# Performance work log

Measured on AMD Instinct MI355X. Metric: run time of the kernel, lower is better.

## Reference

```python
import jax, jax.numpy as jnp
import numpy as np

EPS = 1e-12  # matches torch.nn.functional.normalize default eps

def _l2_normalize(x):
    # F.normalize: x / max(||x||_2, eps)
    n = jnp.sqrt(jnp.sum(x * x, axis=-1, keepdims=True))
    return x / jnp.maximum(n, EPS)

def setup_inputs() -> dict:
    key = jax.random.key(0)
    k1, k2, k3, k4, k5 = jax.random.split(key, 5)
    B, N, D, V = 2048, 50000, 256, 256
    return {
        "query": jax.random.normal(k1, (B, D), dtype=jnp.float32),
        "W": jax.random.normal(k2, (D, D), dtype=jnp.float32) * (1.0 / np.sqrt(D)),
        "b": jax.random.normal(k3, (D,), dtype=jnp.float32) * 0.01,
        "keys": jax.random.normal(k4, (N, D), dtype=jnp.float32),
        "values": jax.random.normal(k5, (N, V), dtype=jnp.float32),
        "usage": jnp.ones((N,), dtype=jnp.float32),
        "top_k": 8,
    }

def reference(query, W, b, keys, values, usage, top_k):
    # q = Linear(query)  (store is full: n_stored == capacity, so no padding branch)
    q = query @ W.T + b                      # (B, D)
    q_norm = _l2_normalize(q)                # (B, D)
    k_norm = _l2_normalize(keys)             # (N, D)
    sim = q_norm @ k_norm.T                  # (B, N) cosine similarity
    scores, indices = jax.lax.top_k(sim, top_k)   # (B, K), (B, K)
    retrieved_values = values[indices]       # (B, K, V) gather
    # usage counter update: +1 per retrieved index (duplicates accumulate)
    usage_new = usage.at[indices.reshape(-1)].add(1.0)
    return retrieved_values, scores, usage_new
```

## Files before the change

### kernel.cpp

```cpp
#include <hip/hip_runtime.h>

#define D 256
#define NKEYS 50000
#define KCHUNK 256
#define NCHUNK 196
#define NKPAD (KCHUNK * NCHUNK)
#define BQ 2048
#define NC (NCHUNK * 4)
#define NCAND 16
#define DNEG_INF (-1.0e300)

typedef __attribute__((ext_vector_type(8))) __bf16 bf16x8;
typedef __attribute__((ext_vector_type(16))) float f32x16;

__device__ __forceinline__ unsigned short f2bf(float x) {
  unsigned int u = __float_as_uint(x);
  unsigned int r = (u + 0x7fffu + ((u >> 16) & 1u)) >> 16;
  return (unsigned short)r;
}

__global__ __launch_bounds__(256) void prep_kernel(const float* __restrict__ query,
                                                   const float* __restrict__ W,
                                                   const float* __restrict__ b,
                                                   const float* __restrict__ keys,
                                                   const float* __restrict__ usage,
                                                   unsigned short* __restrict__ qbf,
                                                   double* __restrict__ q64n,
                                                   double* __restrict__ kinv64,
                                                   unsigned short* __restrict__ kbf,
                                                   float* __restrict__ out_u) {
  __shared__ __align__(16) float As[8][20];
  __shared__ __align__(16) float Bs[256][20];
  if (blockIdx.x < 256) {
    const int tid = threadIdx.x;
    const int qt = tid >> 5;
    const int nt = tid & 31;
    const int m0 = blockIdx.x * 8;

    double acc[8];
#pragma unroll
    for (int j = 0; j < 8; j++) acc[j] = 0.0;

    for (int k0 = 0; k0 < D; k0 += 16) {
      if (tid < 32) {
        int r = tid >> 2, f = tid & 3;
        *(float4*)(&As[r][f * 4]) = *(const float4*)(&query[(m0 + r) * D + k0 + f * 4]);
      }
#pragma unroll
      for (int i = 0; i < 4; i++) {
        int r = (tid >> 2) + 64 * i, f = tid & 3;
        *(float4*)(&Bs[r][f * 4]) = *(const float4*)(&W[r * D + k0 + f * 4]);
      }
      __syncthreads();
#pragma unroll
      for (int kk = 0; kk < 16; kk += 4) {
        float4 af = *(const float4*)(&As[qt][kk]);
#pragma unroll
        for (int j = 0; j < 8; j++) {
          float4 bf = *(const float4*)(&Bs[nt + 32 * j][kk]);
          acc[j] = fma((double)af.x, (double)bf.x, acc[j]);
          acc[j] = fma((double)af.y, (double)bf.y, acc[j]);
          acc[j] = fma((double)af.z, (double)bf.z, acc[j]);
          acc[j] = fma((double)af.w, (double)bf.w, acc[j]);
        }
      }
      __syncthreads();
    }
#pragma unroll
    for (int j = 0; j < 8; j++) acc[j] += (double)b[nt + 32 * j];

    double s = 0.0;
#pragma unroll
    for (int j = 0; j < 8; j++) s = fma(acc[j], acc[j], s);
#pragma unroll
    for (int m = 16; m; m >>= 1) s += __shfl_xor(s, m, 32);
    double den = fmax(sqrt(s), 1e-12);
    int row = m0 + qt;
#pragma unroll
    for (int j = 0; j < 8; j++) {
      double v = acc[j] / den;
      q64n[row * D + nt + 32 * j] = v;
      qbf[row * D + nt + 32 * j] = f2bf((float)v);
    }
  } else {
    int wave = threadIdx.x >> 6, lane = threadIdx.x & 63;
    int r = (blockIdx.x - 256) * 4 + wave;
    if (r >= NKPAD) return;
    if (lane == 0 && r < NKEYS) out_u[r] = usage[r];
    int e = lane * 4;
    int e2 = e ^ ((r & 31) << 3);
    unsigned short* dst = kbf + (long long)r * D + e2;
    if (r >= NKEYS) {
      ushort4 z = {0, 0, 0, 0};
      *(ushort4*)dst = z;
      return;
    }
    float4 v = *(const float4*)(&keys[(long long)r * D + e]);
    double s = (double)v.x * v.x + (double)v.y * v.y + (double)v.z * v.z + (double)v.w * v.w;
#pragma unroll
    for (int m = 32; m; m >>= 1) s += __shfl_xor(s, m, 64);
    double inv = 1.0 / fmax(sqrt(s), 1e-12);
    if (lane == 0) kinv64[r] = inv;
    float fi = (float)inv;
    ushort4 o;
    o.x = f2bf(v.x * fi); o.y = f2bf(v.y * fi); o.z = f2bf(v.z * fi); o.w = f2bf(v.w * fi);
    *(ushort4*)dst = o;
  }
}

__global__ __launch_bounds__(256, 4) void sim_mfma_kernel(const unsigned short* __restrict__ qbf,
                                                          const unsigned short* __restrict__ kbf,
                                                          unsigned int* __restrict__ cand_p) {
  __shared__ __align__(16) unsigned char klds[2][16384];
  const int bid = blockIdx.x;
  const int k8 = bid & 7;
  const int ii = bid >> 3;
  const int qt = ii & 15;
  const int chunk = (ii >> 4) * 8 + k8;
  if (chunk >= NCHUNK) return;
  const int n0 = chunk * KCHUNK;
  const int m0 = qt * 128;

  const int tid = threadIdx.x;
  const int w = tid >> 6;
  const int l = tid & 63;
  const int col = l & 31;
  const int hi = l >> 5;
  const int qrow = m0 + w * 32 + col;

  bf16x8 qf[16];
#pragma unroll
  for (int ks = 0; ks < 16; ks++)
    qf[ks] = *(const bf16x8*)(qbf + (long long)qrow * D + ks * 16 + hi * 8);

  unsigned int s0 = 0u, s1 = 0u, s2 = 0u, s3 = 0u;
  const bool edge = (n0 + KCHUNK > NKEYS);
  const int rbase = col * 512 + hi * 16;
  const int swz = col << 4;
  const char* kchunk = (const char*)kbf + (long long)n0 * 512;

  auto prefetch = [&](unsigned char* buf, int kst) {
#pragma unroll
    for (int i = 0; i < 4; i++) {
      int dstbase = i * 4096 + w * 1024;
      int off = dstbase + l * 16;
      const void* src = kchunk + (long long)(kst * 32 + (off >> 9)) * 512 + (off & 511);
      __builtin_amdgcn_global_load_lds(src, (void*)(buf + dstbase), 16, 0, 0);
    }
  };

  auto compute = [&](const unsigned char* buf, int st) {
    f32x16 acc;
#pragma unroll
    for (int r = 0; r < 16; r++) acc[r] = 0.f;
#pragma unroll
    for (int ks = 0; ks < 16; ks++) {
      bf16x8 a = *(const bf16x8*)(buf + ((rbase + ks * 32) ^ swz));
      acc = __builtin_amdgcn_mfma_f32_32x32x16_bf16(a, qf[ks], acc, 0, 0, 0);
    }
#pragma unroll
    for (int r = 0; r < 16; r++) {
      unsigned int u = __float_as_uint(acc[r] + 2.0f);
      int slot = st * 32 + (r & 3) + 8 * (r >> 2) + 4 * hi;
      unsigned int v = (u & 0xFFFFFF00u) | (unsigned)slot;
      if (edge && (n0 + slot >= NKEYS)) v = 0u;
      unsigned int a0 = min(s0, v); s0 = max(s0, v);
      unsigned int a1 = min(s1, a0); s1 = max(s1, a0);
      unsigned int a2 = min(s2, a1); s2 = max(s2, a1);
      s3 = max(s3, a2);
    }
  };

  prefetch(&klds[0][0], 0);
  __syncthreads();

#pragma unroll 1
  for (int st = 0; st < 8; st += 2) {
    prefetch(&klds[1][0], st + 1);
    compute(&klds[0][0], st);
    __syncthreads();
    if (st + 2 < 8) prefetch(&klds[0][0], st + 2);
    compute(&klds[1][0], st + 1);
    __syncthreads();
  }

  unsigned int b0 = (unsigned int)__shfl_xor((int)s0, 32, 64);
  unsigned int b1 = (unsigned int)__shfl_xor((int)s1, 32, 64);
  unsigned int b2 = (unsigned int)__shfl_xor((int)s2, 32, 64);
  unsigned int b3 = (unsigned int)__shfl_xor((int)s3, 32, 64);
  unsigned int t0 = max(s0, b3), t1 = max(s1, b2), t2 = max(s2, b1), t3 = max(s3, b0);
  unsigned int u0 = max(t0, t2), u2 = min(t0, t2), u1 = max(t1, t3), u3 = min(t1, t3);
  unsigned int w0 = max(u0, u1), w1 = min(u0, u1), w2 = max(u2, u3), w3 = min(u2, u3);

  if (hi == 0) {
    uint4 o = {w0, w1, w2, w3};
    long long base = (long long)qrow * NC + chunk * 4;
    *(uint4*)(cand_p + base) = o;
  }
}

__global__ __launch_bounds__(256) void finalize_kernel(const unsigned int* __restrict__ cand_p,
                                                       const double* __restrict__ q64n,
                                                       const float* __restrict__ keys,
                                                       const double* __restrict__ kinv64,
                                                       const float* __restrict__ values,
                                                       float* __restrict__ scores_out,
                                                       float* __restrict__ out_rv,
                                                       float* __restrict__ usage_out) {
  const int q = blockIdx.x;
  const int tid = threadIdx.x;
  __shared__ int    cidx[NCAND];
  __shared__ double sc[NCAND];
  __shared__ double s8[8];
  __shared__ int    f8[8];

  if (tid < 64) {
    const int lane = tid;
    unsigned int lv[13];
    int li[13];
#pragma unroll
    for (int s = 0; s < 13; s++) {
      int c = lane + 64 * s;
      if (c < NC) {
        unsigned int p = cand_p[(long long)q * NC + c];
        lv[s] = p;
        li[s] = (c >> 2) * KCHUNK + (int)(p & 255u);
      } else { lv[s] = 0u; li[s] = 0x7fffffff; }
    }
#pragma unroll 1
    for (int r = 0; r < NCAND; r++) {
      unsigned int bv = 0u;
      int bi = 0x7fffffff;
#pragma unroll
      for (int s = 0; s < 13; s++)
        if (lv[s] > bv || (lv[s] == bv && li[s] < bi)) { bv = lv[s]; bi = li[s]; }
#pragma unroll
      for (int m = 32; m; m >>= 1) {
        unsigned int ov = (unsigned int)__shfl_xor((int)bv, m, 64);
        int oi = __shfl_xor(bi, m, 64);
        if (ov > bv || (ov == bv && oi < bi)) { bv = ov; bi = oi; }
      }
      if (lane == r) cidx[r] = bi;
#pragma unroll
      for (int s = 0; s < 13; s++)
        if (li[s] == bi) lv[s] = 0u;
    }
  }
  __syncthreads();

  {
    const int g = tid >> 4, ll = tid & 15;
    int idx = cidx[g];
    double s = 0.0;
    const double* qrow = &q64n[(long long)q * D + ll * 16];
    const float* krow = &keys[(long long)idx * D + ll * 16];
#pragma unroll
    for (int t = 0; t < 16; t++) s = fma(qrow[t], (double)krow[t], s);
#pragma unroll
    for (int m = 8; m; m >>= 1) s += __shfl_xor(s, m, 16);
    if (ll == 0) sc[g] = s * kinv64[idx];
  }
  __syncthreads();

  if (tid == 0) {
#pragma unroll 1
    for (int r = 0; r < 8; r++) {
      double bv = DNEG_INF;
      int bi = 0x7fffffff, bg = -1;
#pragma unroll
      for (int t = 0; t < NCAND; t++) {
        if (sc[t] > bv || (sc[t] == bv && cidx[t] < bi)) { bv = sc[t]; bi = cidx[t]; bg = t; }
      }
      s8[r] = bv; f8[r] = bi;
      sc[bg] = DNEG_INF;
    }
  }
  __syncthreads();
  if (tid < 8) {
    scores_out[q * 8 + tid] = (float)s8[tid];
    atomicAdd(&usage_out[f8[tid]], 1.0f);
  }

  {
    const int row = tid >> 5;
    const int c0 = (tid & 31) * 8;
    int idx = f8[row];
    float4 v0 = *(const float4*)(&values[(long long)idx * D + c0]);
    float4 v1 = *(const float4*)(&values[(long long)idx * D + c0 + 4]);
    long long obase = ((long long)q * 8 + row) * D + c0;
    *(float4*)(&out_rv[obase]) = v0;
    *(float4*)(&out_rv[obase + 4]) = v1;
  }
}

extern "C" void kernel_launch(void* const* d_in, const int* in_sizes, int n_in,
                              void* d_out, int out_size, void* d_ws, size_t ws_size,
                              hipStream_t stream) {
  (void)in_sizes; (void)n_in; (void)out_size; (void)ws_size;
  const float* query  = (const float*)d_in[0];
  const float* W      = (const float*)d_in[1];
  const float* b      = (const float*)d_in[2];
  const float* keys   = (const float*)d_in[3];
  const float* values = (const float*)d_in[4];
  const float* usage  = (const float*)d_in[5];

  float* out    = (float*)d_out;
  float* out_rv = out;
  float* out_sc = out + BQ * 8 * D;
  float* out_us = out_sc + BQ * 8;

  double*         q64n   = (double*)d_ws;
  double*         kinv64 = q64n + BQ * D;
  unsigned short* qbf    = (unsigned short*)(kinv64 + NKEYS);
  unsigned short* kbf    = qbf + BQ * D;
  unsigned int*   cand_p = (unsigned int*)(kbf + (long long)NKPAD * D);

  hipLaunchKernelGGL(prep_kernel, dim3(256 + NKPAD / 4), dim3(256), 0, stream,
                     query, W, b, keys, usage, qbf, q64n, kinv64, kbf, out_us);
  hipLaunchKernelGGL(sim_mfma_kernel, dim3(3200), dim3(256), 0, stream, qbf, kbf, cand_p);
  hipLaunchKernelGGL(finalize_kernel, dim3(BQ), dim3(256), 0, stream, cand_p, q64n, keys, kinv64, values, out_sc, out_rv, out_us);
}
```

Before: 163.1 us.

## Use med3 top-4 insertion and split candidate selection across two waves

Replaces the min/max insertion network for each lane's running top-4 with v_med3_u32 operations, which shortens the dependency chain in the hot similarity loop. In finalize, candidate selection now runs on two wavefronts, each picking 12 from half of the chunk candidates, for 24 candidates in total. Each wave does fewer serial reduction rounds over fewer registers. The fp64 rescoring is remapped to 8 threads per candidate so it covers 24 candidates, which adds rescoring work. Picking a per-half top 12 instead of a global top 16 changes which candidates reach the exact rescoring step.

```diff
diff --git a/kernel.cpp b/kernel.cpp
--- a/kernel.cpp
+++ b/kernel.cpp
@@ -7,7 +7,7 @@
 #define NKPAD (KCHUNK * NCHUNK)
 #define BQ 2048
 #define NC (NCHUNK * 4)
-#define NCAND 16
+#define NCAND 24
 #define DNEG_INF (-1.0e300)
 
 typedef __attribute__((ext_vector_type(8))) __bf16 bf16x8;
@@ -17,6 +17,12 @@
   unsigned int u = __float_as_uint(x);
   unsigned int r = (u + 0x7fffu + ((u >> 16) & 1u)) >> 16;
   return (unsigned short)r;
+}
+
+__device__ __forceinline__ unsigned int med3u(unsigned int a, unsigned int b, unsigned int c) {
+  unsigned int d;
+  asm("v_med3_u32 %0, %1, %2, %3" : "=v"(d) : "v"(a), "v"(b), "v"(c));
+  return d;
 }
 
 __global__ __launch_bounds__(256) void prep_kernel(const float* __restrict__ query,
@@ -164,10 +170,11 @@
       int slot = st * 32 + (r & 3) + 8 * (r >> 2) + 4 * hi;
       unsigned int v = (u & 0xFFFFFF00u) | (unsigned)slot;
       if (edge && (n0 + slot >= NKEYS)) v = 0u;
-      unsigned int a0 = min(s0, v); s0 = max(s0, v);
-      unsigned int a1 = min(s1, a0); s1 = max(s1, a0);
-      unsigned int a2 = min(s2, a1); s2 = max(s2, a1);
-      s3 = max(s3, a2);
+      unsigned int n1 = med3u(s0, s1, v);
+      unsigned int n2 = med3u(s1, s2, v);
+      unsigned int n3 = med3u(s2, s3, v);
+      s0 = max(s0, v);
+      s1 = n1; s2 = n2; s3 = n3;
     }
   };
 
@@ -214,25 +221,28 @@
   __shared__ double s8[8];
   __shared__ int    f8[8];
 
-  if (tid < 64) {
-    const int lane = tid;
-    unsigned int lv[13];
-    int li[13];
-#pragma unroll
-    for (int s = 0; s < 13; s++) {
+  if (tid < 128) {
+    const int half = tid >> 6;
+    const int lane = tid & 63;
+    const int base = half * 392;
+    unsigned int lv[7];
+    int li[7];
+#pragma unroll
+    for (int s = 0; s < 7; s++) {
       int c = lane + 64 * s;
-      if (c < NC) {
-        unsigned int p = cand_p[(long long)q * NC + c];
+      if (c < 392) {
+        int cg = base + c;
+        unsigned int p = cand_p[(long long)q * NC + cg];
         lv[s] = p;
-        li[s] = (c >> 2) * KCHUNK + (int)(p & 255u);
+        li[s] = (cg >> 2) * KCHUNK + (int)(p & 255u);
       } else { lv[s] = 0u; li[s] = 0x7fffffff; }
     }
 #pragma unroll 1
-    for (int r = 0; r < NCAND; r++) {
+    for (int r = 0; r < 12; r++) {
       unsigned int bv = 0u;
       int bi = 0x7fffffff;
 #pragma unroll
-      for (int s = 0; s < 13; s++)
+      for (int s = 0; s < 7; s++)
         if (lv[s] > bv || (lv[s] == bv && li[s] < bi)) { bv = lv[s]; bi = li[s]; }
 #pragma unroll
       for (int m = 32; m; m >>= 1) {
@@ -240,25 +250,27 @@
         int oi = __shfl_xor(bi, m, 64);
         if (ov > bv || (ov == bv && oi < bi)) { bv = ov; bi = oi; }
       }
-      if (lane == r) cidx[r] = bi;
-#pragma unroll
-      for (int s = 0; s < 13; s++)
+      if (lane == r) cidx[half * 12 + r] = bi;
+#pragma unroll
+      for (int s = 0; s < 7; s++)
         if (li[s] == bi) lv[s] = 0u;
     }
   }
   __syncthreads();
 
   {
-    const int g = tid >> 4, ll = tid & 15;
-    int idx = cidx[g];
-    double s = 0.0;
-    const double* qrow = &q64n[(long long)q * D + ll * 16];
-    const float* krow = &keys[(long long)idx * D + ll * 16];
-#pragma unroll
-    for (int t = 0; t < 16; t++) s = fma(qrow[t], (double)krow[t], s);
-#pragma unroll
-    for (int m = 8; m; m >>= 1) s += __shfl_xor(s, m, 16);
-    if (ll == 0) sc[g] = s * kinv64[idx];
+    const int g = tid >> 3, ll = tid & 7;
+    if (g < NCAND) {
+      int idx = cidx[g];
+      double s = 0.0;
+      const double* qrow = &q64n[(long long)q * D + ll * 32];
+      const float* krow = &keys[(long long)idx * D + ll * 32];
+#pragma unroll
+      for (int t = 0; t < 32; t++) s = fma(qrow[t], (double)krow[t], s);
+#pragma unroll
+      for (int m = 4; m; m >>= 1) s += __shfl_xor(s, m, 8);
+      if (ll == 0) sc[g] = s * kinv64[idx];
+    }
   }
   __syncthreads();
 
```

Result: faster. 159.6 us (-2.1%).

## Use med3 top-4 insertion, fold bias into MFMA init, one wave per query in finalize

Applied to the files above, without the earlier changes.

In the similarity kernel, the +2.0 bias now seeds the MFMA accumulator instead of being added afterward. The per-element top-4 insertion network is rewritten with v_med3_u32, cutting the min/max chain to three med3 plus one max. The finalize kernel now gives each wave one query instead of a full 256-thread block, so four queries share a block. Candidate selection, double-precision rescoring, rank-based top-8 ordering and the value gather all stay within that wave using shuffles, which removes most shared-memory traffic, block syncs and the serial single-thread sort. The trade-off is higher register pressure (32 doubles per lane) and more shuffle work per wave.

```diff
diff --git a/kernel.cpp b/kernel.cpp
--- a/kernel.cpp
+++ b/kernel.cpp
@@ -17,6 +17,12 @@
   unsigned int u = __float_as_uint(x);
   unsigned int r = (u + 0x7fffu + ((u >> 16) & 1u)) >> 16;
   return (unsigned short)r;
+}
+
+__device__ __forceinline__ unsigned int med3u(unsigned int a, unsigned int b, unsigned int c) {
+  unsigned int d;
+  asm("v_med3_u32 %0, %1, %2, %3" : "=v"(d) : "v"(a), "v"(b), "v"(c));
+  return d;
 }
 
 __global__ __launch_bounds__(256) void prep_kernel(const float* __restrict__ query,
@@ -152,7 +158,7 @@
   auto compute = [&](const unsigned char* buf, int st) {
     f32x16 acc;
 #pragma unroll
-    for (int r = 0; r < 16; r++) acc[r] = 0.f;
+    for (int r = 0; r < 16; r++) acc[r] = 2.0f;
 #pragma unroll
     for (int ks = 0; ks < 16; ks++) {
       bf16x8 a = *(const bf16x8*)(buf + ((rbase + ks * 32) ^ swz));
@@ -160,14 +166,15 @@
     }
 #pragma unroll
     for (int r = 0; r < 16; r++) {
-      unsigned int u = __float_as_uint(acc[r] + 2.0f);
+      unsigned int u = __float_as_uint(acc[r]);
       int slot = st * 32 + (r & 3) + 8 * (r >> 2) + 4 * hi;
       unsigned int v = (u & 0xFFFFFF00u) | (unsigned)slot;
       if (edge && (n0 + slot >= NKEYS)) v = 0u;
-      unsigned int a0 = min(s0, v); s0 = max(s0, v);
-      unsigned int a1 = min(s1, a0); s1 = max(s1, a0);
-      unsigned int a2 = min(s2, a1); s2 = max(s2, a1);
-      s3 = max(s3, a2);
+      unsigned int n1 = med3u(s0, s1, v);
+      unsigned int n2 = med3u(s1, s2, v);
+      unsigned int n3 = med3u(s2, s3, v);
+      s0 = max(s0, v);
+      s1 = n1; s2 = n2; s3 = n3;
     }
   };
 
@@ -207,89 +214,87 @@
                                                        float* __restrict__ scores_out,
                                                        float* __restrict__ out_rv,
                                                        float* __restrict__ usage_out) {
-  const int q = blockIdx.x;
-  const int tid = threadIdx.x;
-  __shared__ int    cidx[NCAND];
-  __shared__ double sc[NCAND];
-  __shared__ double s8[8];
-  __shared__ int    f8[8];
-
-  if (tid < 64) {
-    const int lane = tid;
-    unsigned int lv[13];
-    int li[13];
-#pragma unroll
-    for (int s = 0; s < 13; s++) {
-      int c = lane + 64 * s;
-      if (c < NC) {
-        unsigned int p = cand_p[(long long)q * NC + c];
-        lv[s] = p;
-        li[s] = (c >> 2) * KCHUNK + (int)(p & 255u);
-      } else { lv[s] = 0u; li[s] = 0x7fffffff; }
-    }
+  __shared__ int f8s[4][8];
+  const int wv = threadIdx.x >> 6;
+  const int l = threadIdx.x & 63;
+  const int q = blockIdx.x * 4 + wv;
+
+  unsigned int lv[13];
+  int li[13];
+#pragma unroll
+  for (int s = 0; s < 13; s++) {
+    int c = l + 64 * s;
+    if (c < NC) {
+      unsigned int p = cand_p[(long long)q * NC + c];
+      lv[s] = p;
+      li[s] = (c >> 2) * KCHUNK + (int)(p & 255u);
+    } else { lv[s] = 0u; li[s] = 0x7fffffff; }
+  }
+  int myidx = 0;
 #pragma unroll 1
-    for (int r = 0; r < NCAND; r++) {
-      unsigned int bv = 0u;
-      int bi = 0x7fffffff;
-#pragma unroll
-      for (int s = 0; s < 13; s++)
-        if (lv[s] > bv || (lv[s] == bv && li[s] < bi)) { bv = lv[s]; bi = li[s]; }
-#pragma unroll
-      for (int m = 32; m; m >>= 1) {
-        unsigned int ov = (unsigned int)__shfl_xor((int)bv, m, 64);
-        int oi = __shfl_xor(bi, m, 64);
-        if (ov > bv || (ov == bv && oi < bi)) { bv = ov; bi = oi; }
-      }
-      if (lane == r) cidx[r] = bi;
-#pragma unroll
-      for (int s = 0; s < 13; s++)
-        if (li[s] == bi) lv[s] = 0u;
-    }
+  for (int r = 0; r < NCAND; r++) {
+    unsigned int bv = 0u;
+    int bi = 0x7fffffff;
+#pragma unroll
+    for (int s = 0; s < 13; s++)
+      if (lv[s] > bv || (lv[s] == bv && li[s] < bi)) { bv = lv[s]; bi = li[s]; }
+#pragma unroll
+    for (int m = 32; m; m >>= 1) {
+      unsigned int ov = (unsigned int)__shfl_xor((int)bv, m, 64);
+      int oi = __shfl_xor(bi, m, 64);
+      if (ov > bv || (ov == bv && oi < bi)) { bv = ov; bi = oi; }
+    }
+    if (l == r) myidx = bi;
+#pragma unroll
+    for (int s = 0; s < 13; s++)
+      if (li[s] == bi) lv[s] = 0u;
+  }
+
+  const int sub = l & 7;
+  const double* qr = &q64n[(long long)q * D + sub * 32];
+  double qv[32];
+#pragma unroll
+  for (int t = 0; t < 32; t++) qv[t] = qr[t];
+  double scp[2];
+#pragma unroll 1
+  for (int p = 0; p < 2; p++) {
+    int cand = p * 8 + (l >> 3);
+    int idx = __shfl(myidx, cand, 64);
+    const float* kr = &keys[(long long)idx * D + sub * 32];
+    double s = 0.0;
+#pragma unroll
+    for (int t = 0; t < 32; t++) s = fma(qv[t], (double)kr[t], s);
+#pragma unroll
+    for (int m = 4; m; m >>= 1) s += __shfl_xor(s, m, 8);
+    scp[p] = s * kinv64[idx];
+  }
+
+  double a0 = __shfl(scp[0], (l & 7) * 8, 64);
+  double a1 = __shfl(scp[1], (l & 7) * 8, 64);
+  double myv = (l < 8) ? a0 : a1;
+  int rank = 0;
+#pragma unroll
+  for (int t = 0; t < NCAND; t++) {
+    double tv = __shfl(myv, t, 64);
+    int ti = __shfl(myidx, t, 64);
+    if (tv > myv || (tv == myv && ti < myidx)) rank++;
+  }
+  if (l < NCAND && rank < 8) {
+    scores_out[q * 8 + rank] = (float)myv;
+    atomicAdd(&usage_out[myidx], 1.0f);
+    f8s[wv][rank] = myidx;
   }
   __syncthreads();
 
   {
-    const int g = tid >> 4, ll = tid & 15;
-    int idx = cidx[g];
-    double s = 0.0;
-    const double* qrow = &q64n[(long long)q * D + ll * 16];
-    const float* krow = &keys[(long long)idx * D + ll * 16];
-#pragma unroll
-    for (int t = 0; t < 16; t++) s = fma(qrow[t], (double)krow[t], s);
-#pragma unroll
-    for (int m = 8; m; m >>= 1) s += __shfl_xor(s, m, 16);
-    if (ll == 0) sc[g] = s * kinv64[idx];
-  }
-  __syncthreads();
-
-  if (tid == 0) {
-#pragma unroll 1
-    for (int r = 0; r < 8; r++) {
-      double bv = DNEG_INF;
-      int bi = 0x7fffffff, bg = -1;
-#pragma unroll
-      for (int t = 0; t < NCAND; t++) {
-        if (sc[t] > bv || (sc[t] == bv && cidx[t] < bi)) { bv = sc[t]; bi = cidx[t]; bg = t; }
-      }
-      s8[r] = bv; f8[r] = bi;
-      sc[bg] = DNEG_INF;
-    }
-  }
-  __syncthreads();
-  if (tid < 8) {
-    scores_out[q * 8 + tid] = (float)s8[tid];
-    atomicAdd(&usage_out[f8[tid]], 1.0f);
-  }
-
-  {
-    const int row = tid >> 5;
-    const int c0 = (tid & 31) * 8;
-    int idx = f8[row];
-    float4 v0 = *(const float4*)(&values[(long long)idx * D + c0]);
-    float4 v1 = *(const float4*)(&values[(long long)idx * D + c0 + 4]);
-    long long obase = ((long long)q * 8 + row) * D + c0;
-    *(float4*)(&out_rv[obase]) = v0;
-    *(float4*)(&out_rv[obase + 4]) = v1;
+    const int row = l >> 3;
+    const int c0 = sub * 32;
+    int idx = f8s[wv][row];
+    const float* vr = &values[(long long)idx * D + c0];
+    float* orow = &out_rv[((long long)q * 8 + row) * D + c0];
+#pragma unroll
+    for (int t = 0; t < 8; t++)
+      *(float4*)(&orow[t * 4]) = *(const float4*)(&vr[t * 4]);
   }
 }
 
@@ -318,5 +323,5 @@
   hipLaunchKernelGGL(prep_kernel, dim3(256 + NKPAD / 4), dim3(256), 0, stream,
                      query, W, b, keys, usage, qbf, q64n, kinv64, kbf, out_us);
   hipLaunchKernelGGL(sim_mfma_kernel, dim3(3200), dim3(256), 0, stream, qbf, kbf, cand_p);
-  hipLaunchKernelGGL(finalize_kernel, dim3(BQ), dim3(256), 0, stream, cand_p, q64n, keys, kinv64, values, out_sc, out_rv, out_us);
-}
+  hipLaunchKernelGGL(finalize_kernel, dim3(BQ / 4), dim3(256), 0, stream, cand_p, q64n, keys, kinv64, values, out_sc, out_rv, out_us);
+}
```

New measurement: 131.1 us (median of 3 runs). -19.6%, faster.
